# Performance work log

Measured on AMD Instinct MI355X. Metric: run time of the kernel, lower is better.

Reference implementation:

```python
import jax, jax.numpy as jnp
import numpy as np

P = 500000   # num optimizee params
H = 64       # hidden size
EPS = 1e-5

def _ln(x, g, b):
    # LayerNorm1D: unbiased std, eps added to std (matches torch .std())
    m = jnp.mean(x, axis=1, keepdims=True)
    s = jnp.std(x, axis=1, keepdims=True, ddof=1)
    return (x - m) / (s + EPS) * g + b

def _lstm_cell(x, hx, cx, Wi, bi, Wh, bh, gi, bgi, gh, bgh, gc, bc):
    z = _ln(x @ Wi.T + bi, gi, bgi) + _ln(hx @ Wh.T + bh, gh, bgh)  # [B,4H]
    i, f, o, g = jnp.split(z, 4, axis=1)
    cx = jax.nn.sigmoid(f) * cx + jax.nn.sigmoid(i) * jnp.tanh(g)
    hx = jax.nn.sigmoid(o) * jnp.tanh(_ln(cx, gc, bc))
    return hx, cx

def setup_inputs() -> dict:
    key = jax.random.key(0)
    ks = jax.random.split(key, 16)
    def n(k, shape, scale=0.05):
        return jax.random.normal(k, shape, dtype=jnp.float32) * scale
    ones = lambda s: jnp.ones(s, jnp.float32)
    zeros = lambda s: jnp.zeros(s, jnp.float32)
    inp = {
        'x': jax.random.normal(ks[0], (P,), dtype=jnp.float32),
        'W1': n(ks[1], (H, 1)), 'b1': zeros((H,)),
        'g1': ones((H,)), 'be1': zeros((H,)),
        'l0_Wi': n(ks[2], (4 * H, H)), 'l0_bi': zeros((4 * H,)),
        'l0_Wh': n(ks[3], (4 * H, H)), 'l0_bh': zeros((4 * H,)),
        'l0_gi': ones((4 * H,)), 'l0_bgi': zeros((4 * H,)),
        'l0_gh': ones((4 * H,)), 'l0_bgh': zeros((4 * H,)),
        'l0_gc': ones((H,)), 'l0_bc': zeros((H,)),
        'l1_Wi': n(ks[4], (4 * H, H)), 'l1_bi': zeros((4 * H,)),
        'l1_Wh': n(ks[5], (4 * H, H)), 'l1_bh': zeros((4 * H,)),
        'l1_gi': ones((4 * H,)), 'l1_bgi': zeros((4 * H,)),
        'l1_gh': ones((4 * H,)), 'l1_bgh': zeros((4 * H,)),
        'l1_gc': ones((H,)), 'l1_bc': zeros((H,)),
        'Wo': n(ks[6], (1, H)), 'bo': zeros((1,)),
    }
    return inp

def reference(x, W1, b1, g1, be1,
              l0_Wi, l0_bi, l0_Wh, l0_bh, l0_gi, l0_bgi, l0_gh, l0_bgh, l0_gc, l0_bc,
              l1_Wi, l1_bi, l1_Wh, l1_bh, l1_gi, l1_bgi, l1_gh, l1_bgh, l1_gc, l1_bc,
              Wo, bo):
    # AdaptiveMetaLearner.forward: append mean grad -> batch B = P+1
    xb = jnp.concatenate([x, jnp.mean(x)[None]])[:, None]        # [B,1]
    h = jnp.tanh(_ln(xb @ W1.T + b1, g1, be1))                    # [B,H]
    B = h.shape[0]
    hx = cx = jnp.zeros((B, H), h.dtype)
    hx, cx = _lstm_cell(h, hx, cx, l0_Wi, l0_bi, l0_Wh, l0_bh,
                        l0_gi, l0_bgi, l0_gh, l0_bgh, l0_gc, l0_bc)
    h2x = c2x = jnp.zeros((B, H), h.dtype)
    h2x, c2x = _lstm_cell(hx, h2x, c2x, l1_Wi, l1_bi, l1_Wh, l1_bh,
                          l1_gi, l1_bgi, l1_gh, l1_bgh, l1_gc, l1_bc)
    out = h2x @ Wo.T + bo                                         # [B,1]
    return out[:-1], out[-1:]                                     # (x_out [P,1], qt [1,1])
```

## Files before the change

kernel.cpp:

```cpp
#include <hip/hip_runtime.h>

#define EPS 1e-5f

typedef __attribute__((ext_vector_type(8))) short bf16x8;
typedef __attribute__((ext_vector_type(4))) short short4v;
typedef __attribute__((ext_vector_type(4))) float f32x4;

__device__ __forceinline__ float fexp(float x){ return __builtin_amdgcn_exp2f(x*1.4426950408889634f); }
__device__ __forceinline__ float frcp(float x){ return __builtin_amdgcn_rcpf(x); }
__device__ __forceinline__ float fsig(float x){ return frcp(1.0f + fexp(-x)); }
__device__ __forceinline__ float ftanh(float x){ return 1.0f - 2.0f*frcp(fexp(2.0f*x) + 1.0f); }

__device__ __forceinline__ short bfhi(float v){ return (short)(__float_as_uint(v) >> 16); }
__device__ __forceinline__ float bfhif(float v){ return __uint_as_float(__float_as_uint(v) & 0xFFFF0000u); }

#define WS_NEED (2048*4 + 2*16384*2)

__global__ void mean_part(const float* __restrict__ x, int P, float* __restrict__ part)
{
    __shared__ float red[256];
    int tid = blockIdx.x*256 + threadIdx.x;
    float s = 0.0f;
    for (int i = tid; i < P; i += 256*1024) s += x[i];
    red[threadIdx.x] = s; __syncthreads();
    for (int w = 128; w > 0; w >>= 1){
        if (threadIdx.x < w) red[threadIdx.x] += red[threadIdx.x + w];
        __syncthreads();
    }
    if (threadIdx.x == 0) part[blockIdx.x] = red[0];
}

__global__ void mean_fin(const float* __restrict__ part, float* __restrict__ ws, int P)
{
    __shared__ float red[1024];
    int t = threadIdx.x;
    red[t] = part[t]; __syncthreads();
    for (int w = 512; w > 0; w >>= 1){
        if (t < w) red[t] += red[t + w];
        __syncthreads();
    }
    if (t == 0) ws[0] = red[0] / (float)P;
}

__global__ void precomp_add(
    const float* __restrict__ bh0, const float* __restrict__ gh0,
    const float* __restrict__ bgh0, const float* __restrict__ bgi0,
    const float* __restrict__ bh1, const float* __restrict__ gh1,
    const float* __restrict__ bgh1, const float* __restrict__ bgi1,
    float* __restrict__ ws)
{
    const int l = blockIdx.x;
    const float* bh  = l ? bh1  : bh0;
    const float* gh  = l ? gh1  : gh0;
    const float* bgh = l ? bgh1 : bgh0;
    const float* bgi = l ? bgi1 : bgi0;
    float* add = ws + 1056 + l*256;
    int t = threadIdx.x;

    __shared__ float r1[256], r2[256];
    float v = bh[t];
    r1[t] = v; r2[t] = v*v; __syncthreads();
    for (int w = 128; w > 0; w >>= 1){
        if (t < w){ r1[t] += r1[t+w]; r2[t] += r2[t+w]; }
        __syncthreads();
    }
    float m   = r1[0] * (1.0f/256.0f);
    float var = (r2[0] - 256.0f*m*m) * (1.0f/255.0f);
    float s   = sqrtf(fmaxf(var, 0.0f));
    float c   = (v - m) * frcp(s + EPS) * gh[t] + bgh[t];
    add[t] = c + bgi[t];
}

__global__ void precomp_wlo(const float* __restrict__ Wi0, const float* __restrict__ Wi1,
                            float* __restrict__ ws)
{
    const int l = blockIdx.x;
    const float* Wi = l ? Wi1 : Wi0;
    short* wlos = (short*)(ws + 2048) + l*16384;
    int t = threadIdx.x;
    for (int i = 0; i < 8; ++i){
        int slot = i*256 + t;
        int lane = slot & 63, mtks = slot >> 6;
        int mt = mtks >> 1, ks = mtks & 1;
        int g  = (mt << 4) + (lane & 15);
        int k  = (ks << 5) + ((lane >> 4) << 3);
        short tmp[8];
        #pragma unroll
        for (int j = 0; j < 8; ++j){
            float w = Wi[(g << 6) + k + j];
            tmp[j] = bfhi(w - bfhif(w));
        }
        short4v a = { tmp[0], tmp[1], tmp[2], tmp[3] };
        short4v b = { tmp[4], tmp[5], tmp[6], tmp[7] };
        *(short4v*)(wlos + slot*8)     = a;
        *(short4v*)(wlos + slot*8 + 4) = b;
    }
}

struct LayerParams { const float *bi, *gi, *addv, *gc, *bc; };

__global__ __launch_bounds__(256, 3) void fwd_stream(
    const float* __restrict__ x,
    const float* __restrict__ W1, const float* __restrict__ b1,
    const float* __restrict__ g1, const float* __restrict__ be1,
    const float* __restrict__ Wi0, const float* __restrict__ bi0,
    const float* __restrict__ gi0, const float* __restrict__ gc0, const float* __restrict__ bc0,
    const float* __restrict__ Wi1, const float* __restrict__ bi1,
    const float* __restrict__ gi1, const float* __restrict__ gc1, const float* __restrict__ bc1,
    const float* __restrict__ Wo, const float* __restrict__ bo,
    const float* __restrict__ ws, float* __restrict__ out, int P)
{
    __shared__ short wl[16384];
    __shared__ short hb[8192];

    const int tid  = threadIdx.x;
    const int wid  = tid >> 6;
    const int lane = tid & 63;
    const int c16  = lane & 15;
    const int q    = lane >> 4;
    const int row  = blockIdx.x*64 + wid*16 + c16;
    short* hbw = hb + wid*2048;
    const int swz = (c16 & 7) << 3;
    const short* SB = (const short*)(ws + 2048);

    auto stage_hi = [&](const float* __restrict__ W){
        #pragma unroll
        for (int i = 0; i < 16; ++i){
            int idx = i*256 + tid;
            int g = idx >> 4, k0 = (idx & 15) << 2;
            f32x4 w4 = *(const f32x4*)(W + (idx << 2));
            int si = ((g << 6) + k0) ^ ((g & 7) << 3);
            short4v hi = { bfhi(w4[0]), bfhi(w4[1]), bfhi(w4[2]), bfhi(w4[3]) };
            *(short4v*)(wl + si) = hi;
        }
    };

    stage_hi(Wi0);

    float xv = 0.0f;
    if (row < P) xv = x[row];
    else if (row == P) xv = ws[0];

    {
        float h[16];
        float sm = 0.f, sq = 0.f;
        #pragma unroll
        for (int mt4 = 0; mt4 < 4; ++mt4){
            const f32x4 w14 = *(const f32x4*)(W1 + mt4*16 + (q << 2));
            const f32x4 b14 = *(const f32x4*)(b1 + mt4*16 + (q << 2));
            #pragma unroll
            for (int r = 0; r < 4; ++r){
                float v = xv*w14[r] + b14[r];
                h[mt4*4+r] = v; sm += v; sq += v*v;
            }
        }
        sm += __shfl_xor(sm, 16); sm += __shfl_xor(sm, 32);
        sq += __shfl_xor(sq, 16); sq += __shfl_xor(sq, 32);
        const float m   = sm * (1.0f/64.0f);
        const float var = (sq - 64.0f*m*m) * (1.0f/63.0f);
        const float inv = frcp(sqrtf(fmaxf(var, 0.0f)) + EPS);
        #pragma unroll
        for (int mt4 = 0; mt4 < 4; ++mt4){
            const f32x4 g14  = *(const f32x4*)(g1  + mt4*16 + (q << 2));
            const f32x4 be14 = *(const f32x4*)(be1 + mt4*16 + (q << 2));
            #pragma unroll
            for (int r = 0; r < 4; ++r)
                h[mt4*4+r] = ftanh((h[mt4*4+r]-m)*inv*g14[r] + be14[r]);
        }
        #pragma unroll
        for (int mt4 = 0; mt4 < 4; ++mt4){
            int si = ((c16 << 6) + mt4*16 + (q << 2)) ^ swz;
            float a = h[mt4*4+0], b = h[mt4*4+1], c = h[mt4*4+2], d = h[mt4*4+3];
            short4v hi = { bfhi(a), bfhi(b), bfhi(c), bfhi(d) };
            short4v lo = { bfhi(a-bfhif(a)), bfhi(b-bfhif(b)), bfhi(c-bfhif(c)), bfhi(d-bfhif(d)) };
            *(short4v*)(hbw + si)        = hi;
            *(short4v*)(hbw + 1024 + si) = lo;
        }
    }
    __syncthreads();

    f32x4 acc[16];

    auto do_layer = [&](LayerParams p, const short* __restrict__ wlofrag, bool writeback){
        bf16x8 bhh[2], bhl[2];
        #pragma unroll
        for (int ks = 0; ks < 2; ++ks){
            int si = ((c16 << 6) + ks*32 + (q << 3)) ^ swz;
            bhh[ks] = *(const bf16x8*)(hbw + si);
            bhl[ks] = *(const bf16x8*)(hbw + 1024 + si);
        }
        #pragma unroll
        for (int mt = 0; mt < 16; ++mt)
            acc[mt] = *(const f32x4*)(p.bi + mt*16 + (q << 2));
        #pragma unroll
        for (int mt = 0; mt < 16; ++mt){
            #pragma unroll
            for (int ks = 0; ks < 2; ++ks){
                int si = ((((mt << 4) + c16) << 6) + ks*32 + (q << 3)) ^ swz;
                bf16x8 whi = *(const bf16x8*)(wl + si);
                bf16x8 wlo = *(const bf16x8*)(wlofrag + ((mt*2 + ks) << 9) + (lane << 3));
                acc[mt] = __builtin_amdgcn_mfma_f32_16x16x32_bf16(whi, bhh[ks], acc[mt], 0, 0, 0);
                acc[mt] = __builtin_amdgcn_mfma_f32_16x16x32_bf16(whi, bhl[ks], acc[mt], 0, 0, 0);
                acc[mt] = __builtin_amdgcn_mfma_f32_16x16x32_bf16(wlo, bhh[ks], acc[mt], 0, 0, 0);
            }
        }
        float sm = 0.f, sq = 0.f;
        #pragma unroll
        for (int mt = 0; mt < 16; ++mt){
            #pragma unroll
            for (int r = 0; r < 4; ++r){ float v = acc[mt][r]; sm += v; sq += v*v; }
        }
        sm += __shfl_xor(sm, 16); sm += __shfl_xor(sm, 32);
        sq += __shfl_xor(sq, 16); sq += __shfl_xor(sq, 32);
        const float m   = sm * (1.0f/256.0f);
        const float var = (sq - 256.0f*m*m) * (1.0f/255.0f);
        const float inv = frcp(sqrtf(fmaxf(var, 0.0f)) + EPS);

        #pragma unroll
        for (int mt4 = 0; mt4 < 4; ++mt4){
            const f32x4 giI = *(const f32x4*)(p.gi   +       mt4*16 + (q << 2));
            const f32x4 giO = *(const f32x4*)(p.gi   + 128 + mt4*16 + (q << 2));
            const f32x4 giG = *(const f32x4*)(p.gi   + 192 + mt4*16 + (q << 2));
            const f32x4 adI = *(const f32x4*)(p.addv +       mt4*16 + (q << 2));
            const f32x4 adO = *(const f32x4*)(p.addv + 128 + mt4*16 + (q << 2));
            const f32x4 adG = *(const f32x4*)(p.addv + 192 + mt4*16 + (q << 2));
            #pragma unroll
            for (int r = 0; r < 4; ++r){
                const float i_ = (acc[mt4   ][r]-m)*inv*giI[r] + adI[r];
                const float o_ = (acc[mt4+ 8][r]-m)*inv*giO[r] + adO[r];
                const float g_ = (acc[mt4+12][r]-m)*inv*giG[r] + adG[r];
                acc[mt4   ][r] = fsig(i_) * ftanh(g_);
                acc[mt4+ 8][r] = o_;
            }
        }
        float s2 = 0.f, q2 = 0.f;
        #pragma unroll
        for (int mt4 = 0; mt4 < 4; ++mt4){
            #pragma unroll
            for (int r = 0; r < 4; ++r){ float v = acc[mt4][r]; s2 += v; q2 += v*v; }
        }
        s2 += __shfl_xor(s2, 16); s2 += __shfl_xor(s2, 32);
        q2 += __shfl_xor(q2, 16); q2 += __shfl_xor(q2, 32);
        const float mc = s2 * (1.0f/64.0f);
        const float vc = (q2 - 64.0f*mc*mc) * (1.0f/63.0f);
        const float ic = frcp(sqrtf(fmaxf(vc, 0.0f)) + EPS);
        #pragma unroll
        for (int mt4 = 0; mt4 < 4; ++mt4){
            const f32x4 gc4 = *(const f32x4*)(p.gc + mt4*16 + (q << 2));
            const f32x4 bc4 = *(const f32x4*)(p.bc + mt4*16 + (q << 2));
            #pragma unroll
            for (int r = 0; r < 4; ++r)
                acc[mt4][r] = fsig(acc[mt4+8][r]) * ftanh((acc[mt4][r]-mc)*ic*gc4[r] + bc4[r]);
        }
        if (writeback){
            #pragma unroll
            for (int mt4 = 0; mt4 < 4; ++mt4){
                int si = ((c16 << 6) + mt4*16 + (q << 2)) ^ swz;
                float a = acc[mt4][0], b = acc[mt4][1], c = acc[mt4][2], d = acc[mt4][3];
                short4v hi = { bfhi(a), bfhi(b), bfhi(c), bfhi(d) };
                short4v lo = { bfhi(a-bfhif(a)), bfhi(b-bfhif(b)), bfhi(c-bfhif(c)), bfhi(d-bfhif(d)) };
                *(short4v*)(hbw + si)        = hi;
                *(short4v*)(hbw + 1024 + si) = lo;
            }
        }
    };

    do_layer({bi0, gi0, ws + 1056, gc0, bc0}, SB,          true);
    __syncthreads();
    stage_hi(Wi1);
    __syncthreads();
    do_layer({bi1, gi1, ws + 1312, gc1, bc1}, SB + 16384, false);

    float o = 0.f;
    #pragma unroll
    for (int mt4 = 0; mt4 < 4; ++mt4){
        const f32x4 wo4 = *(const f32x4*)(Wo + mt4*16 + (q << 2));
        #pragma unroll
        for (int r = 0; r < 4; ++r) o += acc[mt4][r]*wo4[r];
    }
    o += __shfl_xor(o, 16); o += __shfl_xor(o, 32);
    if (q == 0 && row <= P) out[row] = o + bo[0];
}

__global__ __launch_bounds__(512, 2) void fwd_lds(
    const float* __restrict__ x,
    const float* __restrict__ W1, const float* __restrict__ b1,
    const float* __restrict__ g1, const float* __restrict__ be1,
    const float* __restrict__ Wi0, const float* __restrict__ bi0,
    const float* __restrict__ gi0, const float* __restrict__ gc0, const float* __restrict__ bc0,
    const float* __restrict__ Wi1, const float* __restrict__ bi1,
    const float* __restrict__ gi1, const float* __restrict__ gc1, const float* __restrict__ bc1,
    const float* __restrict__ Wo, const float* __restrict__ bo,
    const float* __restrict__ ws, float* __restrict__ out, int P)
{
    __shared__ short wl[32768];
    __shared__ short hb[16384];

    const int tid  = threadIdx.x;
    const int wid  = tid >> 6;
    const int lane = tid & 63;
    const int c16  = lane & 15;
    const int q    = lane >> 4;
    const int row  = blockIdx.x*128 + wid*16 + c16;
    short* hbw = hb + wid*2048;
    const int swz = (c16 & 7) << 3;

    auto stage = [&](const float* __restrict__ W){
        #pragma unroll
        for (int i = 0; i < 8; ++i){
            int idx = i*512 + tid;
            int g = idx >> 4, k0 = (idx & 15) << 2;
            f32x4 w4 = *(const f32x4*)(W + (idx << 2));
            int si = ((g << 6) + k0) ^ ((g & 7) << 3);
            short4v hi = { bfhi(w4[0]), bfhi(w4[1]), bfhi(w4[2]), bfhi(w4[3]) };
            short4v lo = { bfhi(w4[0]-bfhif(w4[0])), bfhi(w4[1]-bfhif(w4[1])),
                           bfhi(w4[2]-bfhif(w4[2])), bfhi(w4[3]-bfhif(w4[3])) };
            *(short4v*)(wl + si)         = hi;
            *(short4v*)(wl + 16384 + si) = lo;
        }
    };

    stage(Wi0);

    float xv = 0.0f;
    if (row < P) xv = x[row];
    else if (row == P) xv = ws[0];

    {
        const int cb = q << 4;
        float h[16]; float sm = 0.f, sq = 0.f;
        #pragma unroll
        for (int j = 0; j < 16; ++j){
            float v = xv*W1[cb+j] + b1[cb+j];
            h[j] = v; sm += v; sq += v*v;
        }
        sm += __shfl_xor(sm, 16); sm += __shfl_xor(sm, 32);
        sq += __shfl_xor(sq, 16); sq += __shfl_xor(sq, 32);
        const float m   = sm * (1.0f/64.0f);
        const float var = (sq - 64.0f*m*m) * (1.0f/63.0f);
        const float inv = frcp(sqrtf(fmaxf(var, 0.0f)) + EPS);
        #pragma unroll
        for (int j = 0; j < 16; ++j)
            h[j] = ftanh((h[j]-m)*inv*g1[cb+j] + be1[cb+j]);
        #pragma unroll
        for (int j4 = 0; j4 < 4; ++j4){
            int si = ((c16 << 6) + cb + (j4 << 2)) ^ swz;
            short4v hi = { bfhi(h[j4*4+0]), bfhi(h[j4*4+1]), bfhi(h[j4*4+2]), bfhi(h[j4*4+3]) };
            short4v lo = { bfhi(h[j4*4+0]-bfhif(h[j4*4+0])), bfhi(h[j4*4+1]-bfhif(h[j4*4+1])),
                           bfhi(h[j4*4+2]-bfhif(h[j4*4+2])), bfhi(h[j4*4+3]-bfhif(h[j4*4+3])) };
            *(short4v*)(hbw + si)        = hi;
            *(short4v*)(hbw + 1024 + si) = lo;
        }
    }
    __syncthreads();

    f32x4 acc[16];

    auto do_layer = [&](LayerParams p, bool writeback){
        bf16x8 bhh[2], bhl[2];
        #pragma unroll
        for (int ks = 0; ks < 2; ++ks){
            int si = ((c16 << 6) + ks*32 + (q << 3)) ^ swz;
            bhh[ks] = *(const bf16x8*)(hbw + si);
            bhl[ks] = *(const bf16x8*)(hbw + 1024 + si);
        }
        #pragma unroll
        for (int mt = 0; mt < 16; ++mt)
            acc[mt] = *(const f32x4*)(p.bi + mt*16 + (q << 2));
        #pragma unroll
        for (int mt = 0; mt < 16; ++mt){
            #pragma unroll
            for (int ks = 0; ks < 2; ++ks){
                int si = ((((mt << 4) + c16) << 6) + ks*32 + (q << 3)) ^ swz;
                bf16x8 whi = *(const bf16x8*)(wl + si);
                bf16x8 wlo = *(const bf16x8*)(wl + 16384 + si);
                acc[mt] = __builtin_amdgcn_mfma_f32_16x16x32_bf16(whi, bhh[ks], acc[mt], 0, 0, 0);
                acc[mt] = __builtin_amdgcn_mfma_f32_16x16x32_bf16(whi, bhl[ks], acc[mt], 0, 0, 0);
                acc[mt] = __builtin_amdgcn_mfma_f32_16x16x32_bf16(wlo, bhh[ks], acc[mt], 0, 0, 0);
            }
        }
        float sm = 0.f, sq = 0.f;
        #pragma unroll
        for (int mt = 0; mt < 16; ++mt){
            #pragma unroll
            for (int r = 0; r < 4; ++r){ float v = acc[mt][r]; sm += v; sq += v*v; }
        }
        sm += __shfl_xor(sm, 16); sm += __shfl_xor(sm, 32);
        sq += __shfl_xor(sq, 16); sq += __shfl_xor(sq, 32);
        const float m   = sm * (1.0f/256.0f);
        const float var = (sq - 256.0f*m*m) * (1.0f/255.0f);
        const float inv = frcp(sqrtf(fmaxf(var, 0.0f)) + EPS);

        #pragma unroll
        for (int mt4 = 0; mt4 < 4; ++mt4){
            const f32x4 giI = *(const f32x4*)(p.gi   +       mt4*16 + (q << 2));
            const f32x4 giO = *(const f32x4*)(p.gi   + 128 + mt4*16 + (q << 2));
            const f32x4 giG = *(const f32x4*)(p.gi   + 192 + mt4*16 + (q << 2));
            const f32x4 adI = *(const f32x4*)(p.addv +       mt4*16 + (q << 2));
            const f32x4 adO = *(const f32x4*)(p.addv + 128 + mt4*16 + (q << 2));
            const f32x4 adG = *(const f32x4*)(p.addv + 192 + mt4*16 + (q << 2));
            #pragma unroll
            for (int r = 0; r < 4; ++r){
                const float i_ = (acc[mt4   ][r]-m)*inv*giI[r] + adI[r];
                const float o_ = (acc[mt4+ 8][r]-m)*inv*giO[r] + adO[r];
                const float g_ = (acc[mt4+12][r]-m)*inv*giG[r] + adG[r];
                acc[mt4   ][r] = fsig(i_) * ftanh(g_);
                acc[mt4+ 8][r] = o_;
            }
        }
        float s2 = 0.f, q2 = 0.f;
        #pragma unroll
        for (int mt4 = 0; mt4 < 4; ++mt4){
            #pragma unroll
            for (int r = 0; r < 4; ++r){ float v = acc[mt4][r]; s2 += v; q2 += v*v; }
        }
        s2 += __shfl_xor(s2, 16); s2 += __shfl_xor(s2, 32);
        q2 += __shfl_xor(q2, 16); q2 += __shfl_xor(q2, 32);
        const float mc = s2 * (1.0f/64.0f);
        const float vc = (q2 - 64.0f*mc*mc) * (1.0f/63.0f);
        const float ic = frcp(sqrtf(fmaxf(vc, 0.0f)) + EPS);
        #pragma unroll
        for (int mt4 = 0; mt4 < 4; ++mt4){
            const f32x4 gc4 = *(const f32x4*)(p.gc + mt4*16 + (q << 2));
            const f32x4 bc4 = *(const f32x4*)(p.bc + mt4*16 + (q << 2));
            #pragma unroll
            for (int r = 0; r < 4; ++r)
                acc[mt4][r] = fsig(acc[mt4+8][r]) * ftanh((acc[mt4][r]-mc)*ic*gc4[r] + bc4[r]);
        }
        if (writeback){
            #pragma unroll
            for (int mt4 = 0; mt4 < 4; ++mt4){
                int si = ((c16 << 6) + mt4*16 + (q << 2)) ^ swz;
                float a = acc[mt4][0], b = acc[mt4][1], c = acc[mt4][2], d = acc[mt4][3];
                short4v hi = { bfhi(a), bfhi(b), bfhi(c), bfhi(d) };
                short4v lo = { bfhi(a-bfhif(a)), bfhi(b-bfhif(b)), bfhi(c-bfhif(c)), bfhi(d-bfhif(d)) };
                *(short4v*)(hbw + si)        = hi;
                *(short4v*)(hbw + 1024 + si) = lo;
            }
        }
    };

    do_layer({bi0, gi0, ws + 1056, gc0, bc0}, true);
    __syncthreads();
    stage(Wi1);
    __syncthreads();
    do_layer({bi1, gi1, ws + 1312, gc1, bc1}, false);

    float o = 0.f;
    #pragma unroll
    for (int mt4 = 0; mt4 < 4; ++mt4){
        const f32x4 wo4 = *(const f32x4*)(Wo + mt4*16 + (q << 2));
        #pragma unroll
        for (int r = 0; r < 4; ++r) o += acc[mt4][r]*wo4[r];
    }
    o += __shfl_xor(o, 16); o += __shfl_xor(o, 32);
    if (q == 0 && row <= P) out[row] = o + bo[0];
}

extern "C" void kernel_launch(void* const* d_in, const int* in_sizes, int n_in,
                              void* d_out, int out_size, void* d_ws, size_t ws_size,
                              hipStream_t stream)
{
    (void)n_in; (void)out_size;
    const float* x     = (const float*)d_in[0];
    const float* W1    = (const float*)d_in[1];
    const float* b1    = (const float*)d_in[2];
    const float* g1    = (const float*)d_in[3];
    const float* be1   = (const float*)d_in[4];
    const float* l0_Wi = (const float*)d_in[5];
    const float* l0_bi = (const float*)d_in[6];
    const float* l0_bh = (const float*)d_in[8];
    const float* l0_gi = (const float*)d_in[9];
    const float* l0_bgi= (const float*)d_in[10];
    const float* l0_gh = (const float*)d_in[11];
    const float* l0_bgh= (const float*)d_in[12];
    const float* l0_gc = (const float*)d_in[13];
    const float* l0_bc = (const float*)d_in[14];
    const float* l1_Wi = (const float*)d_in[15];
    const float* l1_bi = (const float*)d_in[16];
    const float* l1_bh = (const float*)d_in[18];
    const float* l1_gi = (const float*)d_in[19];
    const float* l1_bgi= (const float*)d_in[20];
    const float* l1_gh = (const float*)d_in[21];
    const float* l1_bgh= (const float*)d_in[22];
    const float* l1_gc = (const float*)d_in[23];
    const float* l1_bc = (const float*)d_in[24];
    const float* Wo    = (const float*)d_in[25];
    const float* bo    = (const float*)d_in[26];

    int P = in_sizes[0];
    int B = P + 1;
    float* ws  = (float*)d_ws;
    float* out = (float*)d_out;

    mean_part<<<1024, 256, 0, stream>>>(x, P, ws + 16);
    mean_fin<<<1, 1024, 0, stream>>>(ws + 16, ws, P);
    precomp_add<<<2, 256, 0, stream>>>(
        l0_bh, l0_gh, l0_bgh, l0_bgi,
        l1_bh, l1_gh, l1_bgh, l1_bgi, ws);

    if (ws_size >= (size_t)WS_NEED){
        precomp_wlo<<<2, 256, 0, stream>>>(l0_Wi, l1_Wi, ws);
        fwd_stream<<<(B + 63)/64, 256, 0, stream>>>(
            x, W1, b1, g1, be1,
            l0_Wi, l0_bi, l0_gi, l0_gc, l0_bc,
            l1_Wi, l1_bi, l1_gi, l1_gc, l1_bc,
            Wo, bo, ws, out, P);
    } else {
        fwd_lds<<<(B + 127)/128, 512, 0, stream>>>(
            x, W1, b1, g1, be1,
            l0_Wi, l0_bi, l0_gi, l0_gc, l0_bc,
            l1_Wi, l1_bi, l1_gi, l1_gc, l1_bc,
            Wo, bo, ws, out, P);
    }
}
```

Before: 262.0 us.

## Stream both hi and lo weight fragments from global, drop LDS weight staging and barriers

Adds a precompute kernel that packs Wi hi and lo bf16 fragments in MFMA lane order into workspace. A new forward kernel reads both fragments straight from global/L2 instead of staging the hi part in LDS, which removes the weight-staging loops and all block barriers and shrinks LDS to the per-wave h buffer. This should cut LDS traffic and barrier stalls and may raise occupancy, at the cost of more global/L2 load bandwidth per MFMA. The old LDS-only fallback kernel is removed, and the streaming kernel becomes the fallback when the workspace is small.

```diff
diff --git a/kernel.cpp b/kernel.cpp
--- a/kernel.cpp
+++ b/kernel.cpp
@@ -14,7 +14,8 @@
 __device__ __forceinline__ short bfhi(float v){ return (short)(__float_as_uint(v) >> 16); }
 __device__ __forceinline__ float bfhif(float v){ return __uint_as_float(__float_as_uint(v) & 0xFFFF0000u); }
 
-#define WS_NEED (2048*4 + 2*16384*2)
+#define WS_NEED_MIN  (2048*4 + 2*16384*2)
+#define WS_NEED_FULL (2048*4 + 2*32768*2)
 
 __global__ void mean_part(const float* __restrict__ x, int P, float* __restrict__ part)
 {
@@ -69,6 +70,33 @@
     float s   = sqrtf(fmaxf(var, 0.0f));
     float c   = (v - m) * frcp(s + EPS) * gh[t] + bgh[t];
     add[t] = c + bgi[t];
+}
+
+__global__ void precomp_wfrag(const float* __restrict__ Wi0, const float* __restrict__ Wi1,
+                              float* __restrict__ ws)
+{
+    const int l = blockIdx.x;
+    const float* Wi = l ? Wi1 : Wi0;
+    short* wf = (short*)(ws + 2048) + l*32768;
+    int t = threadIdx.x;
+    for (int i = 0; i < 8; ++i){
+        int slot = i*256 + t;
+        int lane = slot & 63, mtks = slot >> 6;
+        int g  = ((mtks >> 1) << 4) + (lane & 15);
+        int k  = ((mtks & 1) << 5) + ((lane >> 4) << 3);
+        short hi8[8], lo8[8];
+        #pragma unroll
+        for (int j = 0; j < 8; ++j){
+            float w = Wi[(g << 6) + k + j];
+            hi8[j] = bfhi(w);
+            lo8[j] = bfhi(w - bfhif(w));
+        }
+        short* d = wf + slot*16;
+        *(short4v*)(d     ) = short4v{ hi8[0], hi8[1], hi8[2], hi8[3] };
+        *(short4v*)(d +  4) = short4v{ hi8[4], hi8[5], hi8[6], hi8[7] };
+        *(short4v*)(d +  8) = short4v{ lo8[0], lo8[1], lo8[2], lo8[3] };
+        *(short4v*)(d + 12) = short4v{ lo8[4], lo8[5], lo8[6], lo8[7] };
+    }
 }
 
 __global__ void precomp_wlo(const float* __restrict__ Wi0, const float* __restrict__ Wi1,
@@ -90,14 +118,174 @@
             float w = Wi[(g << 6) + k + j];
             tmp[j] = bfhi(w - bfhif(w));
         }
-        short4v a = { tmp[0], tmp[1], tmp[2], tmp[3] };
-        short4v b = { tmp[4], tmp[5], tmp[6], tmp[7] };
-        *(short4v*)(wlos + slot*8)     = a;
-        *(short4v*)(wlos + slot*8 + 4) = b;
+        *(short4v*)(wlos + slot*8)     = short4v{ tmp[0], tmp[1], tmp[2], tmp[3] };
+        *(short4v*)(wlos + slot*8 + 4) = short4v{ tmp[4], tmp[5], tmp[6], tmp[7] };
     }
 }
 
 struct LayerParams { const float *bi, *gi, *addv, *gc, *bc; };
+
+__global__ __launch_bounds__(256, 3) void fwd_nobar(
+    const float* __restrict__ x,
+    const float* __restrict__ W1, const float* __restrict__ b1,
+    const float* __restrict__ g1, const float* __restrict__ be1,
+    const float* __restrict__ bi0, const float* __restrict__ gi0,
+    const float* __restrict__ gc0, const float* __restrict__ bc0,
+    const float* __restrict__ bi1, const float* __restrict__ gi1,
+    const float* __restrict__ gc1, const float* __restrict__ bc1,
+    const float* __restrict__ Wo, const float* __restrict__ bo,
+    const float* __restrict__ ws, float* __restrict__ out, int P)
+{
+    __shared__ short hb[8192];
+
+    const int tid  = threadIdx.x;
+    const int wid  = tid >> 6;
+    const int lane = tid & 63;
+    const int c16  = lane & 15;
+    const int q    = lane >> 4;
+    const int row  = blockIdx.x*64 + wid*16 + c16;
+    short* hbw = hb + wid*2048;
+    const int swz = (c16 & 7) << 3;
+    const short* SB = (const short*)(ws + 2048);
+
+    float xv = 0.0f;
+    if (row < P) xv = x[row];
+    else if (row == P) xv = ws[0];
+
+    {
+        float h[16];
+        float sm = 0.f, sq = 0.f;
+        #pragma unroll
+        for (int mt4 = 0; mt4 < 4; ++mt4){
+            const f32x4 w14 = *(const f32x4*)(W1 + mt4*16 + (q << 2));
+            const f32x4 b14 = *(const f32x4*)(b1 + mt4*16 + (q << 2));
+            #pragma unroll
+            for (int r = 0; r < 4; ++r){
+                float v = xv*w14[r] + b14[r];
+                h[mt4*4+r] = v; sm += v; sq += v*v;
+            }
+        }
+        sm += __shfl_xor(sm, 16); sm += __shfl_xor(sm, 32);
+        sq += __shfl_xor(sq, 16); sq += __shfl_xor(sq, 32);
+        const float m   = sm * (1.0f/64.0f);
+        const float var = (sq - 64.0f*m*m) * (1.0f/63.0f);
+        const float inv = frcp(sqrtf(fmaxf(var, 0.0f)) + EPS);
+        #pragma unroll
+        for (int mt4 = 0; mt4 < 4; ++mt4){
+            const f32x4 g14  = *(const f32x4*)(g1  + mt4*16 + (q << 2));
+            const f32x4 be14 = *(const f32x4*)(be1 + mt4*16 + (q << 2));
+            #pragma unroll
+            for (int r = 0; r < 4; ++r)
+                h[mt4*4+r] = ftanh((h[mt4*4+r]-m)*inv*g14[r] + be14[r]);
+        }
+        #pragma unroll
+        for (int mt4 = 0; mt4 < 4; ++mt4){
+            int si = ((c16 << 6) + mt4*16 + (q << 2)) ^ swz;
+            float a = h[mt4*4+0], b = h[mt4*4+1], c = h[mt4*4+2], d = h[mt4*4+3];
+            *(short4v*)(hbw + si)        = short4v{ bfhi(a), bfhi(b), bfhi(c), bfhi(d) };
+            *(short4v*)(hbw + 1024 + si) = short4v{ bfhi(a-bfhif(a)), bfhi(b-bfhif(b)),
+                                                    bfhi(c-bfhif(c)), bfhi(d-bfhif(d)) };
+        }
+    }
+
+    f32x4 acc[16];
+
+    auto do_layer = [&](LayerParams p, const short* __restrict__ wfrag, bool writeback){
+        bf16x8 bhh[2], bhl[2];
+        #pragma unroll
+        for (int ks = 0; ks < 2; ++ks){
+            int si = ((c16 << 6) + ks*32 + (q << 3)) ^ swz;
+            bhh[ks] = *(const bf16x8*)(hbw + si);
+            bhl[ks] = *(const bf16x8*)(hbw + 1024 + si);
+        }
+        #pragma unroll
+        for (int mt = 0; mt < 16; ++mt)
+            acc[mt] = *(const f32x4*)(p.bi + mt*16 + (q << 2));
+        #pragma unroll
+        for (int mt = 0; mt < 16; ++mt){
+            #pragma unroll
+            for (int ks = 0; ks < 2; ++ks){
+                int off = (((mt << 1) + ks) << 10) + (lane << 4);
+                bf16x8 whi = *(const bf16x8*)(wfrag + off);
+                bf16x8 wlo = *(const bf16x8*)(wfrag + off + 8);
+                acc[mt] = __builtin_amdgcn_mfma_f32_16x16x32_bf16(whi, bhh[ks], acc[mt], 0, 0, 0);
+                acc[mt] = __builtin_amdgcn_mfma_f32_16x16x32_bf16(whi, bhl[ks], acc[mt], 0, 0, 0);
+                acc[mt] = __builtin_amdgcn_mfma_f32_16x16x32_bf16(wlo, bhh[ks], acc[mt], 0, 0, 0);
+            }
+        }
+        float sm = 0.f, sq = 0.f;
+        #pragma unroll
+        for (int mt = 0; mt < 16; ++mt){
+            #pragma unroll
+            for (int r = 0; r < 4; ++r){ float v = acc[mt][r]; sm += v; sq += v*v; }
+        }
+        sm += __shfl_xor(sm, 16); sm += __shfl_xor(sm, 32);
+        sq += __shfl_xor(sq, 16); sq += __shfl_xor(sq, 32);
+        const float m   = sm * (1.0f/256.0f);
+        const float var = (sq - 256.0f*m*m) * (1.0f/255.0f);
+        const float inv = frcp(sqrtf(fmaxf(var, 0.0f)) + EPS);
+
+        #pragma unroll
+        for (int mt4 = 0; mt4 < 4; ++mt4){
+            const f32x4 giI = *(const f32x4*)(p.gi   +       mt4*16 + (q << 2));
+            const f32x4 giO = *(const f32x4*)(p.gi   + 128 + mt4*16 + (q << 2));
+            const f32x4 giG = *(const f32x4*)(p.gi   + 192 + mt4*16 + (q << 2));
+            const f32x4 adI = *(const f32x4*)(p.addv +       mt4*16 + (q << 2));
+            const f32x4 adO = *(const f32x4*)(p.addv + 128 + mt4*16 + (q << 2));
+            const f32x4 adG = *(const f32x4*)(p.addv + 192 + mt4*16 + (q << 2));
+            #pragma unroll
+            for (int r = 0; r < 4; ++r){
+                const float i_ = (acc[mt4   ][r]-m)*inv*giI[r] + adI[r];
+                const float o_ = (acc[mt4+ 8][r]-m)*inv*giO[r] + adO[r];
+                const float g_ = (acc[mt4+12][r]-m)*inv*giG[r] + adG[r];
+                acc[mt4   ][r] = fsig(i_) * ftanh(g_);
+                acc[mt4+ 8][r] = o_;
+            }
+        }
+        float s2 = 0.f, q2 = 0.f;
+        #pragma unroll
+        for (int mt4 = 0; mt4 < 4; ++mt4){
+            #pragma unroll
+            for (int r = 0; r < 4; ++r){ float v = acc[mt4][r]; s2 += v; q2 += v*v; }
+        }
+        s2 += __shfl_xor(s2, 16); s2 += __shfl_xor(s2, 32);
+        q2 += __shfl_xor(q2, 16); q2 += __shfl_xor(q2, 32);
+        const float mc = s2 * (1.0f/64.0f);
+        const float vc = (q2 - 64.0f*mc*mc) * (1.0f/63.0f);
+        const float ic = frcp(sqrtf(fmaxf(vc, 0.0f)) + EPS);
+        #pragma unroll
+        for (int mt4 = 0; mt4 < 4; ++mt4){
+            const f32x4 gc4 = *(const f32x4*)(p.gc + mt4*16 + (q << 2));
+            const f32x4 bc4 = *(const f32x4*)(p.bc + mt4*16 + (q << 2));
+            #pragma unroll
+            for (int r = 0; r < 4; ++r)
+                acc[mt4][r] = fsig(acc[mt4+8][r]) * ftanh((acc[mt4][r]-mc)*ic*gc4[r] + bc4[r]);
+        }
+        if (writeback){
+            #pragma unroll
+            for (int mt4 = 0; mt4 < 4; ++mt4){
+                int si = ((c16 << 6) + mt4*16 + (q << 2)) ^ swz;
+                float a = acc[mt4][0], b = acc[mt4][1], c = acc[mt4][2], d = acc[mt4][3];
+                *(short4v*)(hbw + si)        = short4v{ bfhi(a), bfhi(b), bfhi(c), bfhi(d) };
+                *(short4v*)(hbw + 1024 + si) = short4v{ bfhi(a-bfhif(a)), bfhi(b-bfhif(b)),
+                                                        bfhi(c-bfhif(c)), bfhi(d-bfhif(d)) };
+            }
+        }
+    };
+
+    do_layer({bi0, gi0, ws + 1056, gc0, bc0}, SB,          true);
+    do_layer({bi1, gi1, ws + 1312, gc1, bc1}, SB + 32768, false);
+
+    float o = 0.f;
+    #pragma unroll
+    for (int mt4 = 0; mt4 < 4; ++mt4){
+        const f32x4 wo4 = *(const f32x4*)(Wo + mt4*16 + (q << 2));
+        #pragma unroll
+        for (int r = 0; r < 4; ++r) o += acc[mt4][r]*wo4[r];
+    }
+    o += __shfl_xor(o, 16); o += __shfl_xor(o, 32);
+    if (q == 0 && row <= P) out[row] = o + bo[0];
+}
 
 __global__ __launch_bounds__(256, 3) void fwd_stream(
     const float* __restrict__ x,
@@ -130,8 +318,7 @@
             int g = idx >> 4, k0 = (idx & 15) << 2;
             f32x4 w4 = *(const f32x4*)(W + (idx << 2));
             int si = ((g << 6) + k0) ^ ((g & 7) << 3);
-            short4v hi = { bfhi(w4[0]), bfhi(w4[1]), bfhi(w4[2]), bfhi(w4[3]) };
-            *(short4v*)(wl + si) = hi;
+            *(short4v*)(wl + si) = short4v{ bfhi(w4[0]), bfhi(w4[1]), bfhi(w4[2]), bfhi(w4[3]) };
         }
     };
 
@@ -171,10 +358,9 @@
         for (int mt4 = 0; mt4 < 4; ++mt4){
             int si = ((c16 << 6) + mt4*16 + (q << 2)) ^ swz;
             float a = h[mt4*4+0], b = h[mt4*4+1], c = h[mt4*4+2], d = h[mt4*4+3];
-            short4v hi = { bfhi(a), bfhi(b), bfhi(c), bfhi(d) };
-            short4v lo = { bfhi(a-bfhif(a)), bfhi(b-bfhif(b)), bfhi(c-bfhif(c)), bfhi(d-bfhif(d)) };
-            *(short4v*)(hbw + si)        = hi;
-            *(short4v*)(hbw + 1024 + si) = lo;
+            *(short4v*)(hbw + si)        = short4v{ bfhi(a), bfhi(b), bfhi(c), bfhi(d) };
+            *(short4v*)(hbw + 1024 + si) = short4v{ bfhi(a-bfhif(a)), bfhi(b-bfhif(b)),
+                                                    bfhi(c-bfhif(c)), bfhi(d-bfhif(d)) };
         }
     }
     __syncthreads();
@@ -257,10 +443,9 @@
             for (int mt4 = 0; mt4 < 4; ++mt4){
                 int si = ((c16 << 6) + mt4*16 + (q << 2)) ^ swz;
                 float a = acc[mt4][0], b = acc[mt4][1], c = acc[mt4][2], d = acc[mt4][3];
-                short4v hi = { bfhi(a), bfhi(b), bfhi(c), bfhi(d) };
-                short4v lo = { bfhi(a-bfhif(a)), bfhi(b-bfhif(b)), bfhi(c-bfhif(c)), bfhi(d-bfhif(d)) };
-                *(short4v*)(hbw + si)        = hi;
-                *(short4v*)(hbw + 1024 + si) = lo;
+                *(short4v*)(hbw + si)        = short4v{ bfhi(a), bfhi(b), bfhi(c), bfhi(d) };
+                *(short4v*)(hbw + 1024 + si) = short4v{ bfhi(a-bfhif(a)), bfhi(b-bfhif(b)),
+                                                        bfhi(c-bfhif(c)), bfhi(d-bfhif(d)) };
             }
         }
     };
@@ -270,181 +455,6 @@
     stage_hi(Wi1);
     __syncthreads();
     do_layer({bi1, gi1, ws + 1312, gc1, bc1}, SB + 16384, false);
-
-    float o = 0.f;
-    #pragma unroll
-    for (int mt4 = 0; mt4 < 4; ++mt4){
-        const f32x4 wo4 = *(const f32x4*)(Wo + mt4*16 + (q << 2));
-        #pragma unroll
-        for (int r = 0; r < 4; ++r) o += acc[mt4][r]*wo4[r];
-    }
-    o += __shfl_xor(o, 16); o += __shfl_xor(o, 32);
-    if (q == 0 && row <= P) out[row] = o + bo[0];
-}
-
-__global__ __launch_bounds__(512, 2) void fwd_lds(
-    const float* __restrict__ x,
-    const float* __restrict__ W1, const float* __restrict__ b1,
-    const float* __restrict__ g1, const float* __restrict__ be1,
-    const float* __restrict__ Wi0, const float* __restrict__ bi0,
-    const float* __restrict__ gi0, const float* __restrict__ gc0, const float* __restrict__ bc0,
-    const float* __restrict__ Wi1, const float* __restrict__ bi1,
-    const float* __restrict__ gi1, const float* __restrict__ gc1, const float* __restrict__ bc1,
-    const float* __restrict__ Wo, const float* __restrict__ bo,
-    const float* __restrict__ ws, float* __restrict__ out, int P)
-{
-    __shared__ short wl[32768];
-    __shared__ short hb[16384];
-
-    const int tid  = threadIdx.x;
-    const int wid  = tid >> 6;
-    const int lane = tid & 63;
-    const int c16  = lane & 15;
-    const int q    = lane >> 4;
-    const int row  = blockIdx.x*128 + wid*16 + c16;
-    short* hbw = hb + wid*2048;
-    const int swz = (c16 & 7) << 3;
-
-    auto stage = [&](const float* __restrict__ W){
-        #pragma unroll
-        for (int i = 0; i < 8; ++i){
-            int idx = i*512 + tid;
-            int g = idx >> 4, k0 = (idx & 15) << 2;
-            f32x4 w4 = *(const f32x4*)(W + (idx << 2));
-            int si = ((g << 6) + k0) ^ ((g & 7) << 3);
-            short4v hi = { bfhi(w4[0]), bfhi(w4[1]), bfhi(w4[2]), bfhi(w4[3]) };
-            short4v lo = { bfhi(w4[0]-bfhif(w4[0])), bfhi(w4[1]-bfhif(w4[1])),
-                           bfhi(w4[2]-bfhif(w4[2])), bfhi(w4[3]-bfhif(w4[3])) };
-            *(short4v*)(wl + si)         = hi;
-            *(short4v*)(wl + 16384 + si) = lo;
-        }
-    };
-
-    stage(Wi0);
-
-    float xv = 0.0f;
-    if (row < P) xv = x[row];
-    else if (row == P) xv = ws[0];
-
-    {
-        const int cb = q << 4;
-        float h[16]; float sm = 0.f, sq = 0.f;
-        #pragma unroll
-        for (int j = 0; j < 16; ++j){
-            float v = xv*W1[cb+j] + b1[cb+j];
-            h[j] = v; sm += v; sq += v*v;
-        }
-        sm += __shfl_xor(sm, 16); sm += __shfl_xor(sm, 32);
-        sq += __shfl_xor(sq, 16); sq += __shfl_xor(sq, 32);
-        const float m   = sm * (1.0f/64.0f);
-        const float var = (sq - 64.0f*m*m) * (1.0f/63.0f);
-        const float inv = frcp(sqrtf(fmaxf(var, 0.0f)) + EPS);
-        #pragma unroll
-        for (int j = 0; j < 16; ++j)
-            h[j] = ftanh((h[j]-m)*inv*g1[cb+j] + be1[cb+j]);
-        #pragma unroll
-        for (int j4 = 0; j4 < 4; ++j4){
-            int si = ((c16 << 6) + cb + (j4 << 2)) ^ swz;
-            short4v hi = { bfhi(h[j4*4+0]), bfhi(h[j4*4+1]), bfhi(h[j4*4+2]), bfhi(h[j4*4+3]) };
-            short4v lo = { bfhi(h[j4*4+0]-bfhif(h[j4*4+0])), bfhi(h[j4*4+1]-bfhif(h[j4*4+1])),
-                           bfhi(h[j4*4+2]-bfhif(h[j4*4+2])), bfhi(h[j4*4+3]-bfhif(h[j4*4+3])) };
-            *(short4v*)(hbw + si)        = hi;
-            *(short4v*)(hbw + 1024 + si) = lo;
-        }
-    }
-    __syncthreads();
-
-    f32x4 acc[16];
-
-    auto do_layer = [&](LayerParams p, bool writeback){
-        bf16x8 bhh[2], bhl[2];
-        #pragma unroll
-        for (int ks = 0; ks < 2; ++ks){
-            int si = ((c16 << 6) + ks*32 + (q << 3)) ^ swz;
-            bhh[ks] = *(const bf16x8*)(hbw + si);
-            bhl[ks] = *(const bf16x8*)(hbw + 1024 + si);
-        }
-        #pragma unroll
-        for (int mt = 0; mt < 16; ++mt)
-            acc[mt] = *(const f32x4*)(p.bi + mt*16 + (q << 2));
-        #pragma unroll
-        for (int mt = 0; mt < 16; ++mt){
-            #pragma unroll
-            for (int ks = 0; ks < 2; ++ks){
-                int si = ((((mt << 4) + c16) << 6) + ks*32 + (q << 3)) ^ swz;
-                bf16x8 whi = *(const bf16x8*)(wl + si);
-                bf16x8 wlo = *(const bf16x8*)(wl + 16384 + si);
-                acc[mt] = __builtin_amdgcn_mfma_f32_16x16x32_bf16(whi, bhh[ks], acc[mt], 0, 0, 0);
-                acc[mt] = __builtin_amdgcn_mfma_f32_16x16x32_bf16(whi, bhl[ks], acc[mt], 0, 0, 0);
-                acc[mt] = __builtin_amdgcn_mfma_f32_16x16x32_bf16(wlo, bhh[ks], acc[mt], 0, 0, 0);
-            }
-        }
-        float sm = 0.f, sq = 0.f;
-        #pragma unroll
-        for (int mt = 0; mt < 16; ++mt){
-            #pragma unroll
-            for (int r = 0; r < 4; ++r){ float v = acc[mt][r]; sm += v; sq += v*v; }
-        }
-        sm += __shfl_xor(sm, 16); sm += __shfl_xor(sm, 32);
-        sq += __shfl_xor(sq, 16); sq += __shfl_xor(sq, 32);
-        const float m   = sm * (1.0f/256.0f);
-        const float var = (sq - 256.0f*m*m) * (1.0f/255.0f);
-        const float inv = frcp(sqrtf(fmaxf(var, 0.0f)) + EPS);
-
-        #pragma unroll
-        for (int mt4 = 0; mt4 < 4; ++mt4){
-            const f32x4 giI = *(const f32x4*)(p.gi   +       mt4*16 + (q << 2));
-            const f32x4 giO = *(const f32x4*)(p.gi   + 128 + mt4*16 + (q << 2));
-            const f32x4 giG = *(const f32x4*)(p.gi   + 192 + mt4*16 + (q << 2));
-            const f32x4 adI = *(const f32x4*)(p.addv +       mt4*16 + (q << 2));
-            const f32x4 adO = *(const f32x4*)(p.addv + 128 + mt4*16 + (q << 2));
-            const f32x4 adG = *(const f32x4*)(p.addv + 192 + mt4*16 + (q << 2));
-            #pragma unroll
-            for (int r = 0; r < 4; ++r){
-                const float i_ = (acc[mt4   ][r]-m)*inv*giI[r] + adI[r];
-                const float o_ = (acc[mt4+ 8][r]-m)*inv*giO[r] + adO[r];
-                const float g_ = (acc[mt4+12][r]-m)*inv*giG[r] + adG[r];
-                acc[mt4   ][r] = fsig(i_) * ftanh(g_);
-                acc[mt4+ 8][r] = o_;
-            }
-        }
-        float s2 = 0.f, q2 = 0.f;
-        #pragma unroll
-        for (int mt4 = 0; mt4 < 4; ++mt4){
-            #pragma unroll
-            for (int r = 0; r < 4; ++r){ float v = acc[mt4][r]; s2 += v; q2 += v*v; }
-        }
-        s2 += __shfl_xor(s2, 16); s2 += __shfl_xor(s2, 32);
-        q2 += __shfl_xor(q2, 16); q2 += __shfl_xor(q2, 32);
-        const float mc = s2 * (1.0f/64.0f);
-        const float vc = (q2 - 64.0f*mc*mc) * (1.0f/63.0f);
-        const float ic = frcp(sqrtf(fmaxf(vc, 0.0f)) + EPS);
-        #pragma unroll
-        for (int mt4 = 0; mt4 < 4; ++mt4){
-            const f32x4 gc4 = *(const f32x4*)(p.gc + mt4*16 + (q << 2));
-            const f32x4 bc4 = *(const f32x4*)(p.bc + mt4*16 + (q << 2));
-            #pragma unroll
-            for (int r = 0; r < 4; ++r)
-                acc[mt4][r] = fsig(acc[mt4+8][r]) * ftanh((acc[mt4][r]-mc)*ic*gc4[r] + bc4[r]);
-        }
-        if (writeback){
-            #pragma unroll
-            for (int mt4 = 0; mt4 < 4; ++mt4){
-                int si = ((c16 << 6) + mt4*16 + (q << 2)) ^ swz;
-                float a = acc[mt4][0], b = acc[mt4][1], c = acc[mt4][2], d = acc[mt4][3];
-                short4v hi = { bfhi(a), bfhi(b), bfhi(c), bfhi(d) };
-                short4v lo = { bfhi(a-bfhif(a)), bfhi(b-bfhif(b)), bfhi(c-bfhif(c)), bfhi(d-bfhif(d)) };
-                *(short4v*)(hbw + si)        = hi;
-                *(short4v*)(hbw + 1024 + si) = lo;
-            }
-        }
-    };
-
-    do_layer({bi0, gi0, ws + 1056, gc0, bc0}, true);
-    __syncthreads();
-    stage(Wi1);
-    __syncthreads();
-    do_layer({bi1, gi1, ws + 1312, gc1, bc1}, false);
 
     float o = 0.f;
     #pragma unroll
@@ -499,18 +509,19 @@
         l0_bh, l0_gh, l0_bgh, l0_bgi,
         l1_bh, l1_gh, l1_bgh, l1_bgi, ws);
 
-    if (ws_size >= (size_t)WS_NEED){
+    if (ws_size >= (size_t)WS_NEED_FULL){
+        precomp_wfrag<<<2, 256, 0, stream>>>(l0_Wi, l1_Wi, ws);
+        fwd_nobar<<<(B + 63)/64, 256, 0, stream>>>(
+            x, W1, b1, g1, be1,
+            l0_bi, l0_gi, l0_gc, l0_bc,
+            l1_bi, l1_gi, l1_gc, l1_bc,
+            Wo, bo, ws, out, P);
+    } else {
         precomp_wlo<<<2, 256, 0, stream>>>(l0_Wi, l1_Wi, ws);
         fwd_stream<<<(B + 63)/64, 256, 0, stream>>>(
             x, W1, b1, g1, be1,
             l0_Wi, l0_bi, l0_gi, l0_gc, l0_bc,
             l1_Wi, l1_bi, l1_gi, l1_gc, l1_bc,
             Wo, bo, ws, out, P);
-    } else {
-        fwd_lds<<<(B + 127)/128, 512, 0, stream>>>(
-            x, W1, b1, g1, be1,
-            l0_Wi, l0_bi, l0_gi, l0_gc, l0_bc,
-            l1_Wi, l1_bi, l1_gi, l1_gc, l1_bc,
-            Wo, bo, ws, out, P);
-    }
-}
+    }
+}
```

Result: no change. 266.7 us (+1.8%).
